# Kernel optimization log

Measured on AMD Instinct MI355X. Metric: run time of the kernel, lower is better.

## Reference

```python
import jax, jax.numpy as jnp
import numpy as np

NEG_INF = -9e15
ALPHA = 0.2  # LeakyReLU negative slope

N = 8192
D_IN = 512
D_OUT = 256


def setup_inputs() -> dict:
    key = jax.random.key(0)
    k1, k2, k3, k4, k5 = jax.random.split(key, 5)
    features = jax.random.normal(k1, (N, D_IN), dtype=jnp.float32)
    adjacency_matrix = jax.random.randint(k2, (N, N), 0, 2, dtype=jnp.int32)
    # learned params (torch Linear stores [out, in]; we use [in, out] layout)
    s_phi = 1.0 / np.sqrt(D_IN)
    W_phi = jax.random.uniform(k3, (D_IN, D_OUT), jnp.float32, -s_phi, s_phi)
    s_v = 1.0 / np.sqrt(D_OUT)
    w_mu = jax.random.uniform(k4, (D_OUT,), jnp.float32, -s_v, s_v)
    w_xi = jax.random.uniform(k5, (D_OUT,), jnp.float32, -s_v, s_v)
    return {"features": features, "adjacency_matrix": adjacency_matrix,
            "W_phi": W_phi, "w_mu": w_mu, "w_xi": w_xi}


def reference(features, adjacency_matrix, W_phi, w_mu, w_xi):
    h = features @ W_phi                                   # [N, d_out]
    mu = h @ w_mu                                          # [N]
    xi = h @ w_xi                                          # [N]
    e = mu[:, None] + xi[None, :]                          # [N, N] additive scores
    e = jnp.where(e >= 0, e, ALPHA * e)                    # LeakyReLU
    e = jnp.where(adjacency_matrix > 0, e, NEG_INF)        # mask non-edges
    a = jax.nn.softmax(e, axis=1)                          # row softmax (dropout p=0)
    out = a @ h                                            # weighted aggregation
    return jax.nn.elu(out)
```

## Files before the change

kernel.cpp:

```cpp
#include <hip/hip_runtime.h>
#include <cstdint>
#include <cstddef>


#define LOG2E 1.44269504f

typedef __attribute__((ext_vector_type(8))) short short8;
typedef __attribute__((ext_vector_type(4))) float floatx4;

using uint_as1 = __attribute__((address_space(1))) unsigned int;
using uint_as3 = __attribute__((address_space(3))) unsigned int;

__device__ __forceinline__ void gld_lds16(const void* g, void* l) {
  __builtin_amdgcn_global_load_lds((const uint_as1*)g, (uint_as3*)l, 16, 0, 0);
}

__device__ __forceinline__ unsigned short f2b(float f) {
  unsigned u = __float_as_uint(f);
  u += 0x7fffu + ((u >> 16) & 1u);
  return (unsigned short)(u >> 16);
}
__device__ __forceinline__ float b2f(short s) {
  return __uint_as_float(((unsigned)(unsigned short)s) << 16);
}

__global__ void k_bitmaskz(const int* __restrict__ adj,
                           const float* __restrict__ Emu, const float* __restrict__ Fmu,
                           const float* __restrict__ Exi, const float* __restrict__ Fxi,
                           unsigned long long* __restrict__ bm, float* __restrict__ zbuf) {
  int gw = (blockIdx.x * 256 + threadIdx.x) >> 6;
  int lane = threadIdx.x & 63;
  float EM = Emu[gw], FM = Fmu[gw];
  size_t w0 = (size_t)gw * 128;
  float z = 0.f;
  for (int r = 0; r < 128; r += 4) {
    size_t wd = w0 + r;
    int v0 = adj[(wd + 0) * 64 + lane];
    int v1 = adj[(wd + 1) * 64 + lane];
    int v2 = adj[(wd + 2) * 64 + lane];
    int v3 = adj[(wd + 3) * 64 + lane];
    float e0 = Exi[(r + 0) * 64 + lane], f0 = Fxi[(r + 0) * 64 + lane];
    float e1 = Exi[(r + 1) * 64 + lane], f1 = Fxi[(r + 1) * 64 + lane];
    float e2 = Exi[(r + 2) * 64 + lane], f2 = Fxi[(r + 2) * 64 + lane];
    float e3 = Exi[(r + 3) * 64 + lane], f3 = Fxi[(r + 3) * 64 + lane];
    unsigned long long m0 = __ballot(v0 != 0);
    unsigned long long m1 = __ballot(v1 != 0);
    unsigned long long m2 = __ballot(v2 != 0);
    unsigned long long m3 = __ballot(v3 != 0);
    z += (v0 != 0) ? fmaxf(EM * e0, FM * f0) : 0.f;
    z += (v1 != 0) ? fmaxf(EM * e1, FM * f1) : 0.f;
    z += (v2 != 0) ? fmaxf(EM * e2, FM * f2) : 0.f;
    z += (v3 != 0) ? fmaxf(EM * e3, FM * f3) : 0.f;
    if (lane == 0) {
      bm[wd] = m0; bm[wd + 1] = m1; bm[wd + 2] = m2; bm[wd + 3] = m3;
    }
  }
#pragma unroll
  for (int off = 32; off > 0; off >>= 1) z += __shfl_xor(z, off);
  if (lane == 0) zbuf[gw] = z;
}

__global__ void k_cvt_features(const float* __restrict__ f, unsigned short* __restrict__ fb) {
  int tid = blockIdx.x * 256 + threadIdx.x;
  float4 v = ((const float4*)f)[tid];
  ushort4 o = {f2b(v.x), f2b(v.y), f2b(v.z), f2b(v.w)};
  *(ushort4*)&fb[tid * 4] = o;
}

__global__ void k_prep_wt(const float* __restrict__ w, unsigned short* __restrict__ wt) {
  int tid = blockIdx.x * 256 + threadIdx.x;
  int n = tid >> 9, k = tid & 511;
  wt[n * 512 + k] = f2b(w[k * 256 + n]);
}

__global__ void k_prep_p(const float* __restrict__ w, const float* __restrict__ wmu,
                         const float* __restrict__ wxi, float* __restrict__ pmu,
                         float* __restrict__ pxi) {
  int tid = blockIdx.x * 256 + threadIdx.x;
  int k = tid >> 2, seg = tid & 3;
  float sm = 0.f, sx = 0.f;
  int base = k * 256 + seg * 64;
#pragma unroll
  for (int c = 0; c < 64; c += 4) {
    float4 wv = *(const float4*)&w[base + c];
    float4 mv = *(const float4*)&wmu[seg * 64 + c];
    float4 xv = *(const float4*)&wxi[seg * 64 + c];
    sm += wv.x * mv.x + wv.y * mv.y + wv.z * mv.z + wv.w * mv.w;
    sx += wv.x * xv.x + wv.y * xv.y + wv.z * xv.z + wv.w * xv.w;
  }
  sm += __shfl_xor(sm, 1); sm += __shfl_xor(sm, 2);
  sx += __shfl_xor(sx, 1); sx += __shfl_xor(sx, 2);
  if (seg == 0) { pmu[k] = sm; pxi[k] = sx; }
}

__global__ void k_mu_xi(const unsigned short* __restrict__ fb, const float* __restrict__ pmu,
                        const float* __restrict__ pxi, float* __restrict__ Emu,
                        float* __restrict__ Fmu, float* __restrict__ Exi,
                        float* __restrict__ Fxi) {
  int w = threadIdx.x >> 6, l = threadIdx.x & 63;
  int i = blockIdx.x * 4 + w;
  short8 fv = *(const short8*)&fb[i * 512 + l * 8];
  float m = 0.f, x = 0.f;
#pragma unroll
  for (int c = 0; c < 8; ++c) {
    float fvf = b2f(fv[c]);
    m = fmaf(fvf, pmu[l * 8 + c], m);
    x = fmaf(fvf, pxi[l * 8 + c], x);
  }
#pragma unroll
  for (int off = 32; off > 0; off >>= 1) {
    m += __shfl_xor(m, off);
    x += __shfl_xor(x, off);
  }
  if (l == 0) {
    float ms = m * LOG2E, xs = x * LOG2E;
    Emu[i] = __builtin_amdgcn_exp2f(ms);
    Fmu[i] = __builtin_amdgcn_exp2f(0.2f * ms);
    Exi[i] = __builtin_amdgcn_exp2f(xs);
    Fxi[i] = __builtin_amdgcn_exp2f(0.2f * xs);
  }
}

__global__ __launch_bounds__(256, 2) void k_gemm1(const unsigned short* __restrict__ fb,
                                                  const unsigned short* __restrict__ wt,
                                                  unsigned short* __restrict__ ht) {
  __shared__ __align__(16) unsigned short As[64 * 64];
  __shared__ __align__(16) unsigned short Bs[128 * 64];
  int t = threadIdx.x, w = t >> 6, l = t & 63;
  int bm_ = blockIdx.x >> 1, bn = blockIdx.x & 1;
  int m0 = bm_ * 64, n0 = bn * 128;
  int lr = l >> 3, lg = l & 7, g = lg ^ lr;
  int kg = l >> 4, ln = l & 15;
  floatx4 zero = {0.f, 0.f, 0.f, 0.f};
  floatx4 acc[4][2];
#pragma unroll
  for (int mf = 0; mf < 4; ++mf)
#pragma unroll
    for (int nf = 0; nf < 2; ++nf) acc[mf][nf] = zero;

  for (int it = 0; it < 8; ++it) {
    int k0 = it * 64;
#pragma unroll
    for (int q = 0; q < 2; ++q) {
      int row = w * 16 + q * 8 + lr;
      const void* gp = fb + (size_t)(m0 + row) * 512 + k0 + g * 8;
      int lb = __builtin_amdgcn_readfirstlane((w * 16 + q * 8) * 64);
      gld_lds16(gp, &As[lb]);
    }
#pragma unroll
    for (int q = 0; q < 4; ++q) {
      int row = w * 32 + q * 8 + lr;
      const void* gp = wt + (size_t)(n0 + row) * 512 + k0 + g * 8;
      int lb = __builtin_amdgcn_readfirstlane((w * 32 + q * 8) * 64);
      gld_lds16(gp, &Bs[lb]);
    }
    __syncthreads();
#pragma unroll
    for (int ks = 0; ks < 2; ++ks) {
      int gg = ks * 4 + kg;
      int swz = (gg ^ (ln & 7)) * 8;
      short8 bfr[2];
#pragma unroll
      for (int nf = 0; nf < 2; ++nf)
        bfr[nf] = *(const short8*)&Bs[(w * 32 + nf * 16 + ln) * 64 + swz];
#pragma unroll
      for (int mf = 0; mf < 4; ++mf) {
        short8 afr = *(const short8*)&As[(mf * 16 + ln) * 64 + swz];
#pragma unroll
        for (int nf = 0; nf < 2; ++nf)
          acc[mf][nf] = __builtin_amdgcn_mfma_f32_16x16x32_bf16(afr, bfr[nf], acc[mf][nf], 0, 0, 0);
      }
    }
    __syncthreads();
  }
#pragma unroll
  for (int mf = 0; mf < 4; ++mf)
#pragma unroll
    for (int nf = 0; nf < 2; ++nf) {
      int ng = n0 + w * 32 + nf * 16 + ln;
      int mg = m0 + mf * 16 + kg * 4;
      ushort4 o = {f2b(acc[mf][nf][0]), f2b(acc[mf][nf][1]),
                   f2b(acc[mf][nf][2]), f2b(acc[mf][nf][3])};
      *(ushort4*)&ht[(size_t)ng * 8192 + mg] = o;
    }
}

__global__ __launch_bounds__(512, 2) void k_gatt6(const unsigned char* __restrict__ bm8,
                                                  const unsigned short* __restrict__ ht,
                                                  const float* __restrict__ Emu,
                                                  const float* __restrict__ Fmu,
                                                  const float* __restrict__ Exi,
                                                  const float* __restrict__ Fxi,
                                                  float* __restrict__ nump) {
  __shared__ __align__(16) unsigned short Bs[2][256 * 128];
  __shared__ __align__(16) float EfE[1024];
  __shared__ __align__(16) float EfF[1024];

  int t = threadIdx.x, w = t >> 6, l = t & 63;
  int ln = l & 15, kg = l >> 4;
  int jb = blockIdx.x & 7, ig = blockIdx.x >> 3;
  int i0 = ig * 256;
  int jc0 = jb * 1024;

  if (t < 256) {
    *(float4*)&EfE[t * 4] = *(const float4*)&Exi[jc0 + t * 4];
  } else {
    int t2 = t - 256;
    *(float4*)&EfF[t2 * 4] = *(const float4*)&Fxi[jc0 + t2 * 4];
  }

  float EM[2], FM[2];
  const uint4* bprow[2];
#pragma unroll
  for (int mf = 0; mf < 2; ++mf) {
    int i = i0 + w * 32 + mf * 16 + ln;
    EM[mf] = Emu[i];
    FM[mf] = Fmu[i];
    bprow[mf] = (const uint4*)(bm8 + (size_t)i * 1024 + jb * 128);
  }

  floatx4 zero = {0.f, 0.f, 0.f, 0.f};
  floatx4 acc[2][16];
#pragma unroll
  for (int mf = 0; mf < 2; ++mf)
#pragma unroll
    for (int nf = 0; nf < 16; ++nf) acc[mf][nf] = zero;

#define STAGE(win_, b_)                                                       \
  {                                                                           \
    int j0_ = jc0 + (win_) * 128;                                             \
    _Pragma("unroll")                                                         \
    for (int q = 0; q < 8; ++q) {                                             \
      int r0 = w * 32 + q * 4;                                                \
      int row = r0 + (l >> 4);                                                \
      int g = (l & 15) ^ (row & 15);                                          \
      const void* gp = ht + (size_t)row * 8192 + j0_ + g * 8;                 \
      int lb = __builtin_amdgcn_readfirstlane((b_) * (256 * 128) + r0 * 128); \
      gld_lds16(gp, &Bs[0][lb]);                                              \
    }                                                                         \
  }

  uint4 bc[2], bnx[2];
#pragma unroll
  for (int mf = 0; mf < 2; ++mf) bc[mf] = bprow[mf][0];
  STAGE(0, 0);
  __syncthreads();

  for (int win = 0; win < 8; ++win) {
    int buf = win & 1;
    if (win < 7) {
      STAGE(win + 1, buf ^ 1);
#pragma unroll
      for (int mf = 0; mf < 2; ++mf) bnx[mf] = bprow[mf][win + 1];
    }
#pragma unroll
    for (int ksl = 0; ksl < 4; ++ksl) {
      int gran = ksl * 4 + kg;
      int jl = win * 128 + gran * 8;
      float4 e0 = *(const float4*)&EfE[jl];
      float4 e1 = *(const float4*)&EfE[jl + 4];
      float4 f0 = *(const float4*)&EfF[jl];
      float4 f1 = *(const float4*)&EfF[jl + 4];
      float ex[8] = {e0.x, e0.y, e0.z, e0.w, e1.x, e1.y, e1.z, e1.w};
      float fx[8] = {f0.x, f0.y, f0.z, f0.w, f1.x, f1.y, f1.z, f1.w};
      short8 af[2];
#pragma unroll
      for (int mf = 0; mf < 2; ++mf) {
        unsigned word = (ksl == 0) ? bc[mf].x : (ksl == 1) ? bc[mf].y
                      : (ksl == 2) ? bc[mf].z : bc[mf].w;
        unsigned bits = (word >> (kg * 8)) & 0xffu;
        float A = EM[mf], F = FM[mf];
#pragma unroll
        for (int e = 0; e < 8; ++e) {
          float m = fmaxf(A * ex[e], F * fx[e]);
          m = (bits & (1u << e)) ? m : 0.f;
          af[mf][e] = (short)f2b(m);
        }
      }
#pragma unroll
      for (int half = 0; half < 2; ++half) {
        short8 bfv[8];
#pragma unroll
        for (int nf = 0; nf < 8; ++nf) {
          int n = half * 128 + nf * 16 + ln;
          bfv[nf] = *(const short8*)&Bs[buf][n * 128 + ((gran ^ (n & 15)) * 8)];
        }
#pragma unroll
        for (int mf = 0; mf < 2; ++mf)
#pragma unroll
          for (int nf = 0; nf < 8; ++nf)
            acc[mf][half * 8 + nf] = __builtin_amdgcn_mfma_f32_16x16x32_bf16(
                af[mf], bfv[nf], acc[mf][half * 8 + nf], 0, 0, 0);
      }
    }
    __syncthreads();
#pragma unroll
    for (int mf = 0; mf < 2; ++mf) bc[mf] = bnx[mf];
  }
#undef STAGE

  float* np = nump + (size_t)jb * (8192 * 256);
#pragma unroll
  for (int mf = 0; mf < 2; ++mf) {
    int rowb = i0 + w * 32 + mf * 16 + kg * 4;
#pragma unroll
    for (int r = 0; r < 4; ++r) {
      float* rp = np + (size_t)(rowb + r) * 256;
#pragma unroll
      for (int nf = 0; nf < 16; ++nf)
        rp[nf * 16 + ln] = acc[mf][nf][r];
    }
  }
}

__global__ void k_final(const float* __restrict__ nump, const float* __restrict__ zbuf,
                        float* __restrict__ out) {
  int tid = blockIdx.x * 256 + threadIdx.x;
  int i = tid >> 6;
  float zi = 1.0f / zbuf[i];
  float4 v = {0.f, 0.f, 0.f, 0.f};
#pragma unroll
  for (int p = 0; p < 8; ++p) {
    float4 s = *(const float4*)&nump[(size_t)p * (8192 * 256) + tid * 4];
    v.x += s.x; v.y += s.y; v.z += s.z; v.w += s.w;
  }
  v.x *= zi; v.y *= zi; v.z *= zi; v.w *= zi;
  v.x = (v.x > 0.f) ? v.x : (__builtin_amdgcn_exp2f(v.x * LOG2E) - 1.f);
  v.y = (v.y > 0.f) ? v.y : (__builtin_amdgcn_exp2f(v.y * LOG2E) - 1.f);
  v.z = (v.z > 0.f) ? v.z : (__builtin_amdgcn_exp2f(v.z * LOG2E) - 1.f);
  v.w = (v.w > 0.f) ? v.w : (__builtin_amdgcn_exp2f(v.w * LOG2E) - 1.f);
  *(float4*)&out[tid * 4] = v;
}

extern "C" void kernel_launch(void* const* d_in, const int* in_sizes, int n_in,
                              void* d_out, int out_size, void* d_ws, size_t ws_size,
                              hipStream_t stream) {
  const float* features = (const float*)d_in[0];
  const int* adjm = (const int*)d_in[1];
  const float* W_phi = (const float*)d_in[2];
  const float* w_mu = (const float*)d_in[3];
  const float* w_xi = (const float*)d_in[4];
  float* out = (float*)d_out;

  char* ws = (char*)d_ws;
  unsigned short* fb  = (unsigned short*)(ws + 0);
  unsigned short* ht  = (unsigned short*)(ws + 8388608);
  unsigned short* wt  = (unsigned short*)(ws + 12582912);
  float* pmu = (float*)(ws + 12845056);
  float* pxi = (float*)(ws + 12847104);
  float* Emu = (float*)(ws + 12849152);
  float* Fmu = (float*)(ws + 12881920);
  float* Exi = (float*)(ws + 12914688);
  float* Fxi = (float*)(ws + 12947456);
  float* zbuf = (float*)(ws + 12980224);
  unsigned char* bmask = (unsigned char*)(ws + 13631488);
  float* nump = (float*)(ws + 25165824);

  k_cvt_features<<<4096, 256, 0, stream>>>(features, fb);
  k_prep_wt<<<512, 256, 0, stream>>>(W_phi, wt);
  k_prep_p<<<8, 256, 0, stream>>>(W_phi, w_mu, w_xi, pmu, pxi);
  k_mu_xi<<<2048, 256, 0, stream>>>(fb, pmu, pxi, Emu, Fmu, Exi, Fxi);
  k_gemm1<<<256, 256, 0, stream>>>(fb, wt, ht);
  k_bitmaskz<<<2048, 256, 0, stream>>>(adjm, Emu, Fmu, Exi, Fxi,
                                       (unsigned long long*)bmask, zbuf);
  k_gatt6<<<256, 512, 0, stream>>>(bmask, ht, Emu, Fmu, Exi, Fxi, nump);
  k_final<<<2048, 256, 0, stream>>>(nump, zbuf, out);
}
```

Before: 465.7 us.

## Shrink attention block to 128 rows, single-buffer LDS, pack xi factors as bf16 pairs

After: 466.7 us. Within noise of the previous version (+0.2%).

```diff
diff --git a/kernel.cpp b/kernel.cpp
--- a/kernel.cpp
+++ b/kernel.cpp
@@ -185,28 +185,31 @@
     }
 }
 
-__global__ __launch_bounds__(512, 2) void k_gatt6(const unsigned char* __restrict__ bm8,
+__global__ __launch_bounds__(256, 2) void k_gatt7(const unsigned char* __restrict__ bm8,
                                                   const unsigned short* __restrict__ ht,
                                                   const float* __restrict__ Emu,
                                                   const float* __restrict__ Fmu,
                                                   const float* __restrict__ Exi,
                                                   const float* __restrict__ Fxi,
                                                   float* __restrict__ nump) {
-  __shared__ __align__(16) unsigned short Bs[2][256 * 128];
-  __shared__ __align__(16) float EfE[1024];
-  __shared__ __align__(16) float EfF[1024];
+  __shared__ __align__(16) unsigned short Bs[256 * 128];
+  __shared__ __align__(16) unsigned int EfP[1024];
 
   int t = threadIdx.x, w = t >> 6, l = t & 63;
   int ln = l & 15, kg = l >> 4;
   int jb = blockIdx.x & 7, ig = blockIdx.x >> 3;
-  int i0 = ig * 256;
+  int i0 = ig * 128;
   int jc0 = jb * 1024;
 
-  if (t < 256) {
-    *(float4*)&EfE[t * 4] = *(const float4*)&Exi[jc0 + t * 4];
-  } else {
-    int t2 = t - 256;
-    *(float4*)&EfF[t2 * 4] = *(const float4*)&Fxi[jc0 + t2 * 4];
+  {
+    float4 e = *(const float4*)&Exi[jc0 + t * 4];
+    float4 f = *(const float4*)&Fxi[jc0 + t * 4];
+    uint4 p;
+    p.x = (__float_as_uint(f.x) & 0xffff0000u) | (__float_as_uint(e.x) >> 16);
+    p.y = (__float_as_uint(f.y) & 0xffff0000u) | (__float_as_uint(e.y) >> 16);
+    p.z = (__float_as_uint(f.z) & 0xffff0000u) | (__float_as_uint(e.z) >> 16);
+    p.w = (__float_as_uint(f.w) & 0xffff0000u) | (__float_as_uint(e.w) >> 16);
+    *(uint4*)&EfP[t * 4] = p;
   }
 
   float EM[2], FM[2];
@@ -226,30 +229,28 @@
 #pragma unroll
     for (int nf = 0; nf < 16; ++nf) acc[mf][nf] = zero;
 
-#define STAGE(win_, b_)                                                       \
+#define STAGE(win_)                                                           \
   {                                                                           \
     int j0_ = jc0 + (win_) * 128;                                             \
     _Pragma("unroll")                                                         \
-    for (int q = 0; q < 8; ++q) {                                             \
-      int r0 = w * 32 + q * 4;                                                \
+    for (int q = 0; q < 16; ++q) {                                            \
+      int r0 = w * 64 + q * 4;                                                \
       int row = r0 + (l >> 4);                                                \
       int g = (l & 15) ^ (row & 15);                                          \
       const void* gp = ht + (size_t)row * 8192 + j0_ + g * 8;                 \
-      int lb = __builtin_amdgcn_readfirstlane((b_) * (256 * 128) + r0 * 128); \
-      gld_lds16(gp, &Bs[0][lb]);                                              \
+      int lb = __builtin_amdgcn_readfirstlane(r0 * 128);                      \
+      gld_lds16(gp, &Bs[lb]);                                                 \
     }                                                                         \
   }
 
   uint4 bc[2], bnx[2];
 #pragma unroll
   for (int mf = 0; mf < 2; ++mf) bc[mf] = bprow[mf][0];
-  STAGE(0, 0);
+  STAGE(0);
   __syncthreads();
 
   for (int win = 0; win < 8; ++win) {
-    int buf = win & 1;
     if (win < 7) {
-      STAGE(win + 1, buf ^ 1);
 #pragma unroll
       for (int mf = 0; mf < 2; ++mf) bnx[mf] = bprow[mf][win + 1];
     }
@@ -257,12 +258,9 @@
     for (int ksl = 0; ksl < 4; ++ksl) {
       int gran = ksl * 4 + kg;
       int jl = win * 128 + gran * 8;
-      float4 e0 = *(const float4*)&EfE[jl];
-      float4 e1 = *(const float4*)&EfE[jl + 4];
-      float4 f0 = *(const float4*)&EfF[jl];
-      float4 f1 = *(const float4*)&EfF[jl + 4];
-      float ex[8] = {e0.x, e0.y, e0.z, e0.w, e1.x, e1.y, e1.z, e1.w};
-      float fx[8] = {f0.x, f0.y, f0.z, f0.w, f1.x, f1.y, f1.z, f1.w};
+      uint4 p0 = *(const uint4*)&EfP[jl];
+      uint4 p1 = *(const uint4*)&EfP[jl + 4];
+      unsigned pe[8] = {p0.x, p0.y, p0.z, p0.w, p1.x, p1.y, p1.z, p1.w};
       short8 af[2];
 #pragma unroll
       for (int mf = 0; mf < 2; ++mf) {
@@ -272,7 +270,9 @@
         float A = EM[mf], F = FM[mf];
 #pragma unroll
         for (int e = 0; e < 8; ++e) {
-          float m = fmaxf(A * ex[e], F * fx[e]);
+          float Ef = __uint_as_float(pe[e] << 16);
+          float Ff = __uint_as_float(pe[e] & 0xffff0000u);
+          float m = fmaxf(A * Ef, F * Ff);
           m = (bits & (1u << e)) ? m : 0.f;
           af[mf][e] = (short)f2b(m);
         }
@@ -283,7 +283,7 @@
 #pragma unroll
         for (int nf = 0; nf < 8; ++nf) {
           int n = half * 128 + nf * 16 + ln;
-          bfv[nf] = *(const short8*)&Bs[buf][n * 128 + ((gran ^ (n & 15)) * 8)];
+          bfv[nf] = *(const short8*)&Bs[n * 128 + ((gran ^ (n & 15)) * 8)];
         }
 #pragma unroll
         for (int mf = 0; mf < 2; ++mf)
@@ -294,8 +294,12 @@
       }
     }
     __syncthreads();
-#pragma unroll
-    for (int mf = 0; mf < 2; ++mf) bc[mf] = bnx[mf];
+    if (win < 7) {
+      STAGE(win + 1);
+#pragma unroll
+      for (int mf = 0; mf < 2; ++mf) bc[mf] = bnx[mf];
+      __syncthreads();
+    }
   }
 #undef STAGE
 
@@ -363,6 +367,6 @@
   k_gemm1<<<256, 256, 0, stream>>>(fb, wt, ht);
   k_bitmaskz<<<2048, 256, 0, stream>>>(adjm, Emu, Fmu, Exi, Fxi,
                                        (unsigned long long*)bmask, zbuf);
-  k_gatt6<<<256, 512, 0, stream>>>(bmask, ht, Emu, Fmu, Exi, Fxi, nump);
+  k_gatt7<<<512, 256, 0, stream>>>(bmask, ht, Emu, Fmu, Exi, Fxi, nump);
   k_final<<<2048, 256, 0, stream>>>(nump, zbuf, out);
 }
```
